# Performance work log

Hardware: AMD Instinct MI355X
Metric: run time of the kernel (lower is better)

Reference implementation:

```python
import jax, jax.numpy as jnp
import numpy as np

B, G, IN, F, O = 65536, 6, 512, 256, 18


def setup_inputs() -> dict:
    key = jax.random.key(0)
    ks = jax.random.split(key, 9)
    return {
        "state": jax.random.normal(ks[0], (B, IN), dtype=jnp.float32),
        "action": jax.random.randint(ks[1], (B, 1), 0, O, dtype=jnp.int64),
        "idx": jax.random.randint(ks[2], (B,), 0, G, dtype=jnp.int64),
        # per-game expert Linear weights (stored [in, out] so fwd is x @ W)
        "W1": jax.random.normal(ks[3], (G, IN, F), dtype=jnp.float32) * (1.0 / np.sqrt(IN)),
        "b1": jnp.zeros((G, F), dtype=jnp.float32),
        # shared layer
        "W2": jax.random.normal(ks[4], (F, F), dtype=jnp.float32) * (1.0 / np.sqrt(F)),
        "b2": jnp.zeros((F,), dtype=jnp.float32),
        # per-game Q heads
        "Wq": jax.random.normal(ks[5], (G, F, O), dtype=jnp.float32) * (1.0 / np.sqrt(F)),
        "bq": jnp.zeros((G, O), dtype=jnp.float32),
    }


def reference(state, action, idx, W1, b1, W2, b2, Wq, bq):
    # The torch code processes samples grouped by np.unique(idx) and then
    # torch.cat's the groups: this is a stable sort of samples by idx value.
    perm = jnp.argsort(idx)  # jnp.argsort is stable by default
    sp = state[perm]         # [B, IN], samples in group-sorted order
    ip = idx[perm]           # [B]

    # per-game expert: compute all G tiny linears, select the routed one
    h_all = jax.nn.sigmoid(jnp.einsum('bi,gif->bgf', sp, W1) + b1)  # [B,G,F]
    h1 = jnp.take_along_axis(h_all, ip[:, None, None], axis=1)[:, 0, :]  # [B,F]

    # shared layer ('relu' branch)
    h_f = jax.nn.relu(h1 @ W2 + b2)  # [B,F]

    # stacked per-game heads
    q = jnp.tanh(jnp.einsum('bf,gfo->bgo', h_f, Wq) + bq)  # [B,G,O]

    # action gather: q_acted[b,g] = q[b,g,action[b,0]] (action in ORIGINAL order,
    # exactly as in the torch code, which gathers on the permuted-row q)
    a = jnp.broadcast_to(action[:, :1], (B, G))[..., None]  # [B,G,1]
    q_acted = jnp.take_along_axis(q, a, axis=2)[..., 0]     # [B,G]

    # idx gather (again with idx in ORIGINAL order, matching the torch code)
    q_out = jnp.take_along_axis(q_acted, idx[:, None], axis=1)[:, 0]  # [B]
    return q_out
```

## Files before the change

kernel.cpp:

```cpp
#include <hip/hip_runtime.h>
#include <math.h>

#define B_N 65536
#define G_N 6
#define IN_N 512
#define F_N 256
#define O_N 18

#define NB 256
#define CHUNK 256

#define TBM 32
#define MAXT (B_N / TBM + G_N)

typedef __bf16 bf16x8 __attribute__((ext_vector_type(8)));
typedef float f32x4 __attribute__((ext_vector_type(4)));

#define WS_BC     0
#define WS_BOFF   8192
#define WS_NTILES 16448
#define WS_DESC   16512
#define WS_W1F    65536
#define WS_W2F    (WS_W1F + 1572864)
#define WS_WQT    (WS_W2F + 131072)
#define WS_PERM   4194304

__device__ __forceinline__ unsigned short f2bf(float f) {
    union { float f; unsigned u; } a; a.f = f;
    unsigned r = a.u + 0x7fffu + ((a.u >> 16) & 1u);
    return (unsigned short)(r >> 16);
}
__device__ __forceinline__ unsigned pack2(float a, float b) {
    return (unsigned)f2bf(a) | ((unsigned)f2bf(b) << 16);
}
__device__ __forceinline__ bf16x8 asbf(uint4 u) {
    union { uint4 u; bf16x8 b; } c; c.u = u; return c.b;
}

__global__ void k_hist(const int* __restrict__ idx, int* __restrict__ bc) {
    __shared__ int cnt[G_N];
    int t = threadIdx.x;
    if (t < G_N) cnt[t] = 0;
    __syncthreads();
    int e = blockIdx.x * CHUNK + t;
    atomicAdd(&cnt[idx[e]], 1);
    __syncthreads();
    if (t < G_N) bc[blockIdx.x * G_N + t] = cnt[t];
}

__global__ void k_prefix(const int* __restrict__ bc, int* __restrict__ boff,
                         int* __restrict__ ntiles, int* __restrict__ desc) {
    __shared__ int sbc[NB * G_N];
    __shared__ int tot[G_N], st[G_N];
    __shared__ int tstart[G_N + 1];
    int t = threadIdx.x;
    for (int i = t; i < NB * G_N; i += 256) sbc[i] = bc[i];
    __syncthreads();
    int w = t >> 6, l = t & 63;
    for (int g = w; g < G_N; g += 4) {
        int v[4]; int s = 0;
#pragma unroll
        for (int j = 0; j < 4; j++) { v[j] = sbc[(l * 4 + j) * G_N + g]; s += v[j]; }
        int inc = s;
#pragma unroll
        for (int o = 1; o < 64; o <<= 1) { int x = __shfl_up(inc, o, 64); if (l >= o) inc += x; }
        int run = inc - s;
        if (l == 63) tot[g] = inc;
#pragma unroll
        for (int j = 0; j < 4; j++) { sbc[(l * 4 + j) * G_N + g] = run; run += v[j]; }
    }
    __syncthreads();
    if (t == 0) {
        int acc = 0;
        for (int g = 0; g < G_N; g++) { st[g] = acc; acc += tot[g]; }
        int nt = 0;
        for (int g = 0; g < G_N; g++) { tstart[g] = nt; nt += (tot[g] + TBM - 1) / TBM; }
        tstart[G_N] = nt;
        *ntiles = nt;
    }
    __syncthreads();
    for (int i = t; i < NB * G_N; i += 256) boff[i] = sbc[i] + st[i % G_N];
    int nt = tstart[G_N];
    for (int i = t; i < MAXT; i += 256) {
        int gd = 0, r0 = 0, nr = 0;
        if (i < nt) {
            int g = 0;
            while (g < G_N - 1 && i >= tstart[g + 1]) g++;
            int k = i - tstart[g];
            r0 = st[g] + k * TBM;
            int rem = tot[g] - k * TBM;
            nr = rem < TBM ? rem : TBM;
            gd = g;
        }
        desc[i * 3 + 0] = gd; desc[i * 3 + 1] = r0; desc[i * 3 + 2] = nr;
    }
}

__global__ void k_scatter(const int* __restrict__ idx, const int* __restrict__ boff,
                          int* __restrict__ perm) {
    __shared__ int wcnt[4][G_N];
    __shared__ int base[G_N];
    int t = threadIdx.x, w = t >> 6, l = t & 63;
    int e = blockIdx.x * CHUNK + t;
    int g = idx[e];
    int rank = 0;
    for (int gg = 0; gg < G_N; gg++) {
        unsigned long long m = __ballot(g == gg);
        if (g == gg) rank = __popcll(m & ((1ull << l) - 1ull));
        if (l == 0) wcnt[w][gg] = __popcll(m);
    }
    if (t < G_N) base[t] = boff[blockIdx.x * G_N + t];
    __syncthreads();
    int off = base[g] + rank;
    for (int ww = 0; ww < w; ww++) off += wcnt[ww][g];
    perm[off] = e;
}

__global__ void k_pack_all(const float* __restrict__ W1, const float* __restrict__ W2,
                           const float* __restrict__ Wq,
                           unsigned short* __restrict__ W1f, unsigned short* __restrict__ W2f,
                           float* __restrict__ WqT) {
    int kf = blockIdx.x, w = blockIdx.y, z = blockIdx.z;
    if (z == 6 && kf >= 8) {
        int tid = ((kf - 8) * 8 + w) * 128 + threadIdx.x;
        for (int e = tid; e < G_N * O_N * F_N; e += 8192) {
            int f = e & (F_N - 1);
            int go = e >> 8;
            int g = go / O_N, o = go - g * O_N;
            WqT[e] = Wq[((long)g * F_N + f) * O_N + o];
        }
        return;
    }
    const float* src;
    unsigned short* dst;
    int kfTot;
    if (z < 6) { src = W1 + (long)z * IN_N * F_N; dst = W1f + (long)z * IN_N * F_N; kfTot = 16; }
    else       { src = W2; dst = W2f; kfTot = 8; }
    int f = threadIdx.x >> 6, l = threadIdx.x & 63;
    int lrow = l & 15, q = l >> 4;
    int n = w * 32 + f * 16 + lrow;
    int k0 = kf * 32 + q * 8;
    const float* s = src + (long)k0 * F_N + n;
    unsigned o[4];
#pragma unroll
    for (int j = 0; j < 4; j++)
        o[j] = pack2(s[(2 * j) * F_N], s[(2 * j + 1) * F_N]);
    unsigned short* d = dst + ((((long)w * kfTot + kf) * 2 + f) * 64 + l) * 8;
    uint4 v = { o[0], o[1], o[2], o[3] };
    *(uint4*)d = v;
}

__global__ __launch_bounds__(512, 6) void k_fused(
    const float* __restrict__ state, const char* __restrict__ w1f,
    const char* __restrict__ w2f, const float* __restrict__ wqt,
    const float* __restrict__ b1, const float* __restrict__ b2,
    const float* __restrict__ bqv,
    const int* __restrict__ action, const int* __restrict__ idx,
    const int* __restrict__ perm, const int* __restrict__ desc,
    float* __restrict__ out) {
    int td = blockIdx.x;
    int g = desc[td * 3 + 0], row0 = desc[td * 3 + 1], nr = desc[td * 3 + 2];
    if (nr == 0) return;

    __shared__ __align__(16) unsigned short smA[TBM * 512];
    __shared__ float partial[TBM][9];
    __shared__ int gq[TBM], actv[TBM];
    unsigned short* smH = smA;

    int t = threadIdx.x, w = t >> 6, l = t & 63;
    int lrow = l & 15, q = l >> 4;
    int x0 = lrow & 7;

    const char* B1 = w1f + (((long)g * 8 + w) << 15) + l * 16;
    uint4 nb0 = *(const uint4*)(B1);
    uint4 nb1 = *(const uint4*)(B1 + 1024);

    if (t < TBM) {
        int pos = row0 + t; if (pos > B_N - 1) pos = B_N - 1;
        gq[t] = idx[pos];
        actv[t] = action[pos];
    }

    {
        int m = t >> 4, s = t & 15;
        int pr = row0 + m; if (pr > B_N - 1) pr = B_N - 1;
        const float* src = state + (long)perm[pr] * IN_N + s * 4;
        int cb = s >> 1, h = s & 1, mx = m & 7;
        char* rowbase = (char*)smA + m * 1024 + h * 8;
#pragma unroll
        for (int j = 0; j < 8; j++) {
            float4 v = *(const float4*)(src + j * 64);
            uint2 p = { pack2(v.x, v.y), pack2(v.z, v.w) };
            int c = (cb + j * 8) ^ mx;
            *(uint2*)(rowbase + c * 16) = p;
        }
    }
    __syncthreads();

    const char* ar[2];
#pragma unroll
    for (int i = 0; i < 2; i++) ar[i] = (const char*)smA + (i * 16 + lrow) * 1024;

    f32x4 acc[2][2];
#pragma unroll
    for (int i = 0; i < 2; i++)
#pragma unroll
        for (int j = 0; j < 2; j++) acc[i][j] = (f32x4){0.f, 0.f, 0.f, 0.f};

#pragma unroll
    for (int kf = 0; kf < 16; kf++) {
        uint4 cb0 = nb0, cb1 = nb1;
        if (kf < 15) {
            nb0 = *(const uint4*)(B1 + (kf + 1) * 2048);
            nb1 = *(const uint4*)(B1 + (kf + 1) * 2048 + 1024);
        }
        int c = ((kf * 4 + q) ^ x0) * 16;
        bf16x8 af[2];
#pragma unroll
        for (int i = 0; i < 2; i++) af[i] = *(const bf16x8*)(ar[i] + c);
        bf16x8 b0 = asbf(cb0), b1v = asbf(cb1);
#pragma unroll
        for (int i = 0; i < 2; i++) {
            acc[i][0] = __builtin_amdgcn_mfma_f32_16x16x32_bf16(af[i], b0, acc[i][0], 0, 0, 0);
            acc[i][1] = __builtin_amdgcn_mfma_f32_16x16x32_bf16(af[i], b1v, acc[i][1], 0, 0, 0);
        }
    }
    __syncthreads();

    {
        int col0 = w * 32 + lrow;
#pragma unroll
        for (int j = 0; j < 2; j++) {
            int col = col0 + j * 16;
            float bias = b1[g * F_N + col];
            int cc = col >> 3, cb2 = (col & 7) * 2;
#pragma unroll
            for (int i = 0; i < 2; i++)
#pragma unroll
                for (int r = 0; r < 4; r++) {
                    int row = i * 16 + q * 4 + r;
                    float v = acc[i][j][r] + bias;
                    float sg = 1.0f / (1.0f + __expf(-v));
                    int c = cc ^ (row & 7);
                    *(unsigned short*)((char*)smH + row * 512 + c * 16 + cb2) = f2bf(sg);
                }
        }
    }
    __syncthreads();

    const char* B2 = w2f + ((long)w << 14) + l * 16;
    const char* hr[2];
#pragma unroll
    for (int i = 0; i < 2; i++) hr[i] = (const char*)smH + (i * 16 + lrow) * 512;

    f32x4 acc2[2][2];
#pragma unroll
    for (int i = 0; i < 2; i++)
#pragma unroll
        for (int j = 0; j < 2; j++) acc2[i][j] = (f32x4){0.f, 0.f, 0.f, 0.f};

    uint4 m0 = *(const uint4*)(B2);
    uint4 m1 = *(const uint4*)(B2 + 1024);
#pragma unroll
    for (int kf = 0; kf < 8; kf++) {
        uint4 c0 = m0, c1 = m1;
        if (kf < 7) {
            m0 = *(const uint4*)(B2 + (kf + 1) * 2048);
            m1 = *(const uint4*)(B2 + (kf + 1) * 2048 + 1024);
        }
        int c = ((kf * 4 + q) ^ x0) * 16;
        bf16x8 af[2];
#pragma unroll
        for (int i = 0; i < 2; i++) af[i] = *(const bf16x8*)(hr[i] + c);
        bf16x8 b0 = asbf(c0), b1v = asbf(c1);
#pragma unroll
        for (int i = 0; i < 2; i++) {
            acc2[i][0] = __builtin_amdgcn_mfma_f32_16x16x32_bf16(af[i], b0, acc2[i][0], 0, 0, 0);
            acc2[i][1] = __builtin_amdgcn_mfma_f32_16x16x32_bf16(af[i], b1v, acc2[i][1], 0, 0, 0);
        }
    }

    {
        int col0 = w * 32 + lrow;
        float bias0 = b2[col0], bias1 = b2[col0 + 16];
#pragma unroll
        for (int i = 0; i < 2; i++)
#pragma unroll
            for (int r = 0; r < 4; r++) {
                int row = i * 16 + q * 4 + r;
                const float* wp = wqt + ((long)gq[row] * O_N + actv[row]) * F_N;
                float v0 = fmaxf(acc2[i][0][r] + bias0, 0.0f);
                float v1 = fmaxf(acc2[i][1][r] + bias1, 0.0f);
                float s = v0 * wp[col0] + v1 * wp[col0 + 16];
                s += __shfl_xor(s, 1, 64);
                s += __shfl_xor(s, 2, 64);
                s += __shfl_xor(s, 4, 64);
                s += __shfl_xor(s, 8, 64);
                if (lrow == 0) partial[row][w] = s;
            }
    }
    __syncthreads();
    if (t < TBM && t < nr) {
        float s = 0.f;
#pragma unroll
        for (int ww = 0; ww < 8; ww++) s += partial[t][ww];
        out[row0 + t] = tanhf(s + bqv[gq[t] * O_N + actv[t]]);
    }
}

extern "C" void kernel_launch(void* const* d_in, const int* in_sizes, int n_in,
                              void* d_out, int out_size, void* d_ws, size_t ws_size,
                              hipStream_t stream) {
    const float* state  = (const float*)d_in[0];
    const int*   action = (const int*)d_in[1];
    const int*   idx    = (const int*)d_in[2];
    const float* W1     = (const float*)d_in[3];
    const float* b1     = (const float*)d_in[4];
    const float* W2     = (const float*)d_in[5];
    const float* b2     = (const float*)d_in[6];
    const float* Wq     = (const float*)d_in[7];
    const float* bq     = (const float*)d_in[8];
    float* out = (float*)d_out;

    char* ws = (char*)d_ws;
    int* bc      = (int*)(ws + WS_BC);
    int* boff    = (int*)(ws + WS_BOFF);
    int* ntiles  = (int*)(ws + WS_NTILES);
    int* desc    = (int*)(ws + WS_DESC);
    unsigned short* W1f = (unsigned short*)(ws + WS_W1F);
    unsigned short* W2f = (unsigned short*)(ws + WS_W2F);
    float* WqT   = (float*)(ws + WS_WQT);
    int* perm    = (int*)(ws + WS_PERM);

    k_hist<<<NB, CHUNK, 0, stream>>>(idx, bc);
    k_prefix<<<1, 256, 0, stream>>>(bc, boff, ntiles, desc);
    k_scatter<<<NB, CHUNK, 0, stream>>>(idx, boff, perm);
    k_pack_all<<<dim3(16, 8, 7), 128, 0, stream>>>(W1, W2, Wq, W1f, W2f, WqT);
    k_fused<<<MAXT, 512, 0, stream>>>(state, (const char*)W1f, (const char*)W2f, WqT,
                                      b1, b2, bq, action, idx, perm, desc, out);
}
```

Measured before the change: 252.2 us.

## Separate hidden-state LDS buffer, drop barrier, use packed bf16 conversion and fast tanh

Gives the hidden activations their own shared buffer instead of aliasing the input tile. This removes the barrier between the first GEMM and the sigmoid epilogue and lets the W2 fragment prefetch start earlier. It also swaps the manual bf16 rounding for the packed HIP conversion intrinsic, pairs two sigmoid outputs per pack, and uses an exp-based tanh for the output. The cost is more LDS per block, which may limit occupancy, and fast_tanh can produce inf/inf NaN for large inputs.

```diff
diff --git a/kernel.cpp b/kernel.cpp
--- a/kernel.cpp
+++ b/kernel.cpp
@@ -1,4 +1,5 @@
 #include <hip/hip_runtime.h>
+#include <hip/hip_bf16.h>
 #include <math.h>
 
 #define B_N 65536
@@ -25,16 +26,21 @@
 #define WS_WQT    (WS_W2F + 131072)
 #define WS_PERM   4194304
 
+__device__ __forceinline__ unsigned packcvt(float a, float b) {
+    __hip_bfloat162 h = __float22bfloat162_rn(float2{a, b});
+    union { __hip_bfloat162 h; unsigned u; } c; c.h = h; return c.u;
+}
 __device__ __forceinline__ unsigned short f2bf(float f) {
     union { float f; unsigned u; } a; a.f = f;
     unsigned r = a.u + 0x7fffu + ((a.u >> 16) & 1u);
     return (unsigned short)(r >> 16);
 }
-__device__ __forceinline__ unsigned pack2(float a, float b) {
-    return (unsigned)f2bf(a) | ((unsigned)f2bf(b) << 16);
-}
 __device__ __forceinline__ bf16x8 asbf(uint4 u) {
     union { uint4 u; bf16x8 b; } c; c.u = u; return c.b;
+}
+__device__ __forceinline__ float fast_tanh(float x) {
+    float e = __expf(2.0f * x);
+    return 1.0f - 2.0f / (e + 1.0f);
 }
 
 __global__ void k_hist(const int* __restrict__ idx, int* __restrict__ bc) {
@@ -144,7 +150,7 @@
     unsigned o[4];
 #pragma unroll
     for (int j = 0; j < 4; j++)
-        o[j] = pack2(s[(2 * j) * F_N], s[(2 * j + 1) * F_N]);
+        o[j] = packcvt(s[(2 * j) * F_N], s[(2 * j + 1) * F_N]);
     unsigned short* d = dst + ((((long)w * kfTot + kf) * 2 + f) * 64 + l) * 8;
     uint4 v = { o[0], o[1], o[2], o[3] };
     *(uint4*)d = v;
@@ -163,9 +169,9 @@
     if (nr == 0) return;
 
     __shared__ __align__(16) unsigned short smA[TBM * 512];
+    __shared__ __align__(16) unsigned short smH[TBM * 256];
     __shared__ float partial[TBM][9];
     __shared__ int gq[TBM], actv[TBM];
-    unsigned short* smH = smA;
 
     int t = threadIdx.x, w = t >> 6, l = t & 63;
     int lrow = l & 15, q = l >> 4;
@@ -190,7 +196,7 @@
 #pragma unroll
         for (int j = 0; j < 8; j++) {
             float4 v = *(const float4*)(src + j * 64);
-            uint2 p = { pack2(v.x, v.y), pack2(v.z, v.w) };
+            uint2 p = { packcvt(v.x, v.y), packcvt(v.z, v.w) };
             int c = (cb + j * 8) ^ mx;
             *(uint2*)(rowbase + c * 16) = p;
         }
@@ -225,30 +231,34 @@
             acc[i][1] = __builtin_amdgcn_mfma_f32_16x16x32_bf16(af[i], b1v, acc[i][1], 0, 0, 0);
         }
     }
-    __syncthreads();
+
+    const char* B2 = w2f + ((long)w << 14) + l * 16;
+    uint4 m0 = *(const uint4*)(B2);
+    uint4 m1 = *(const uint4*)(B2 + 1024);
 
     {
         int col0 = w * 32 + lrow;
-#pragma unroll
-        for (int j = 0; j < 2; j++) {
-            int col = col0 + j * 16;
-            float bias = b1[g * F_N + col];
-            int cc = col >> 3, cb2 = (col & 7) * 2;
-#pragma unroll
-            for (int i = 0; i < 2; i++)
-#pragma unroll
-                for (int r = 0; r < 4; r++) {
-                    int row = i * 16 + q * 4 + r;
-                    float v = acc[i][j][r] + bias;
-                    float sg = 1.0f / (1.0f + __expf(-v));
-                    int c = cc ^ (row & 7);
-                    *(unsigned short*)((char*)smH + row * 512 + c * 16 + cb2) = f2bf(sg);
-                }
-        }
-    }
-    __syncthreads();
-
-    const char* B2 = w2f + ((long)w << 14) + l * 16;
+        float bias0 = b1[g * F_N + col0];
+        float bias1 = b1[g * F_N + col0 + 16];
+        int cc = col0 >> 3, cb2 = (col0 & 7) * 2;
+#pragma unroll
+        for (int i = 0; i < 2; i++)
+#pragma unroll
+            for (int r = 0; r < 4; r++) {
+                int row = i * 16 + q * 4 + r;
+                float v0 = acc[i][0][r] + bias0;
+                float v1 = acc[i][1][r] + bias1;
+                float sg0 = 1.0f / (1.0f + __expf(-v0));
+                float sg1 = 1.0f / (1.0f + __expf(-v1));
+                unsigned pk = packcvt(sg0, sg1);
+                int rx = row & 7;
+                char* base = (char*)smH + row * 512 + cb2;
+                *(unsigned short*)(base + ((cc)     ^ rx) * 16) = (unsigned short)pk;
+                *(unsigned short*)(base + ((cc + 2) ^ rx) * 16) = (unsigned short)(pk >> 16);
+            }
+    }
+    __syncthreads();
+
     const char* hr[2];
 #pragma unroll
     for (int i = 0; i < 2; i++) hr[i] = (const char*)smH + (i * 16 + lrow) * 512;
@@ -259,8 +269,6 @@
 #pragma unroll
         for (int j = 0; j < 2; j++) acc2[i][j] = (f32x4){0.f, 0.f, 0.f, 0.f};
 
-    uint4 m0 = *(const uint4*)(B2);
-    uint4 m1 = *(const uint4*)(B2 + 1024);
 #pragma unroll
     for (int kf = 0; kf < 8; kf++) {
         uint4 c0 = m0, c1 = m1;
@@ -291,20 +299,20 @@
                 const float* wp = wqt + ((long)gq[row] * O_N + actv[row]) * F_N;
                 float v0 = fmaxf(acc2[i][0][r] + bias0, 0.0f);
                 float v1 = fmaxf(acc2[i][1][r] + bias1, 0.0f);
-                float s = v0 * wp[col0] + v1 * wp[col0 + 16];
-                s += __shfl_xor(s, 1, 64);
-                s += __shfl_xor(s, 2, 64);
-                s += __shfl_xor(s, 4, 64);
-                s += __shfl_xor(s, 8, 64);
-                if (lrow == 0) partial[row][w] = s;
+                float s2 = v0 * wp[col0] + v1 * wp[col0 + 16];
+                s2 += __shfl_xor(s2, 1, 64);
+                s2 += __shfl_xor(s2, 2, 64);
+                s2 += __shfl_xor(s2, 4, 64);
+                s2 += __shfl_xor(s2, 8, 64);
+                if (lrow == 0) partial[row][w] = s2;
             }
     }
     __syncthreads();
     if (t < TBM && t < nr) {
-        float s = 0.f;
-#pragma unroll
-        for (int ww = 0; ww < 8; ww++) s += partial[t][ww];
-        out[row0 + t] = tanhf(s + bqv[gq[t] * O_N + actv[t]]);
+        float s2 = 0.f;
+#pragma unroll
+        for (int ww = 0; ww < 8; ww++) s2 += partial[t][ww];
+        out[row0 + t] = fast_tanh(s2 + bqv[gq[t] * O_N + actv[t]]);
     }
 }
 
```

Measured after the change: 253.4 us. No clear change (+0.4%).
